# Kernel optimization log

Measured on AMD Instinct MI355X. Metric: run time of the kernel, lower is better.

The kernel has to match this reference:

```python
import jax, jax.numpy as jnp
import numpy as np
from jax import lax

EPS = 1e-5  # GroupNorm eps (torch default)

def _silu(x):
    return x * jax.nn.sigmoid(x)

def _conv1x1(x, w, b):
    # x: (N, Ci, H, W), w: (Co, Ci), b: (Co,)
    return jnp.einsum('oi,nihw->nohw', w, x) + b[None, :, None, None]

def _conv3x3(x, w, b):
    # x: (N, Ci, H, W), w: (Co, Ci, 3, 3)
    y = lax.conv_general_dilated(x, w, window_strides=(1, 1), padding='SAME',
                                 dimension_numbers=('NCHW', 'OIHW', 'NCHW'))
    return y + b[None, :, None, None]

def setup_inputs() -> dict:
    key = jax.random.key(0)
    ks = jax.random.split(key, 6)
    B, C, H, W = 32, 512, 64, 64
    cg = 16
    return {
        'x': jax.random.normal(ks[0], (B, C, H, W), dtype=jnp.float32),
        'w1': jax.random.normal(ks[1], (cg, cg), dtype=jnp.float32) * 0.1,
        'b1': jnp.zeros((cg,), jnp.float32),
        'wh': jax.random.normal(ks[2], (cg, cg), dtype=jnp.float32) * 0.1,
        'bh': jnp.zeros((cg,), jnp.float32),
        'ww': jax.random.normal(ks[3], (cg, cg), dtype=jnp.float32) * 0.1,
        'bw': jnp.zeros((cg,), jnp.float32),
        'w3': jax.random.normal(ks[4], (cg, cg, 3, 3), dtype=jnp.float32) * 0.1,
        'b3': jnp.zeros((cg,), jnp.float32),
        'gamma': jnp.ones((cg,), jnp.float32),
        'beta': jnp.zeros((cg,), jnp.float32),
    }

def reference(x, w1, b1, wh, bh, ww, bw, w3, b3, gamma, beta):
    b, c, h, w = x.shape
    cg = w1.shape[0]
    g = c // cg
    n = b * g
    hw = h * w
    xg = x.reshape(n, cg, h, w)
    # directional pooling: (N, cg, H, 1) and (N, cg, W, 1)
    x_h = jnp.mean(xg, axis=3, keepdims=True)
    x_w = jnp.transpose(jnp.mean(xg, axis=2, keepdims=True), (0, 1, 3, 2))
    y = jnp.concatenate([x_h, x_w], axis=2)            # (N, cg, H+W, 1)
    y = _silu(_conv1x1(y, w1, b1))
    y_h, y_w = y[:, :, :h, :], y[:, :, h:, :]
    y_w = jnp.transpose(y_w, (0, 1, 3, 2))             # (N, cg, 1, W)
    a_h = jax.nn.sigmoid(_conv1x1(y_h, wh, bh))        # (N, cg, H, 1)
    a_w = jax.nn.sigmoid(_conv1x1(y_w, ww, bw))        # (N, cg, 1, W)
    x1 = xg * a_h * a_w
    # GroupNorm(num_groups=1): normalize over (cg, H, W) per sample
    mu = jnp.mean(x1, axis=(1, 2, 3), keepdims=True)
    var = jnp.var(x1, axis=(1, 2, 3), keepdims=True)
    x1 = (x1 - mu) * lax.rsqrt(var + EPS)
    x1 = x1 * gamma[None, :, None, None] + beta[None, :, None, None]
    x3 = _silu(_conv3x3(xg, w3, b3))
    A1 = jax.nn.softmax(x1.reshape(n, cg, hw), axis=-1)
    A3 = jax.nn.softmax(x3.reshape(n, cg, hw), axis=-1)
    v1 = jnp.mean(x1, axis=(2, 3))                     # (N, cg)
    v3 = jnp.mean(x3, axis=(2, 3))                     # (N, cg)
    s1 = jnp.einsum('nc,ncp->np', v1, A3)              # (N, HW)
    s2 = jnp.einsum('nc,ncp->np', v3, A1)
    s = jax.nn.sigmoid(s1 + s2).reshape(n, 1, h, w)
    out = (xg * s).reshape(b, c, h, w)
    return out
```

## Files before the change

### kernel.cpp

```cpp
#include <hip/hip_runtime.h>


typedef short bf16x8 __attribute__((ext_vector_type(8)));
typedef short bf16x4 __attribute__((ext_vector_type(4)));
typedef float f32x4 __attribute__((ext_vector_type(4)));

__device__ __forceinline__ unsigned short f2bf(float f) {
    union { float f; unsigned int u; } v; v.f = f;
    unsigned int u = v.u;
    u += 0x7fffu + ((u >> 16) & 1u);
    return (unsigned short)(u >> 16);
}
__device__ __forceinline__ float bf2f(unsigned short h) {
    union { unsigned int u; float f; } v; v.u = ((unsigned int)h) << 16;
    return v.f;
}
__device__ __forceinline__ float sigm(float v) { return 1.0f / (1.0f + __expf(-v)); }

#define XIDX(h1,w1,c) ((((h1)*2 + ((c)>>3))*66 + (w1))*8 + ((c)&7))

__global__ __launch_bounds__(1024) void ema_fused(
    const float* __restrict__ x,
    const float* __restrict__ w1, const float* __restrict__ b1,
    const float* __restrict__ wh, const float* __restrict__ bh,
    const float* __restrict__ ww, const float* __restrict__ bw,
    const float* __restrict__ w3, const float* __restrict__ b3,
    const float* __restrict__ gamma, const float* __restrict__ beta,
    float* __restrict__ out)
{
    const int n    = blockIdx.x;
    const int tid  = threadIdx.x;
    const int lane = tid & 63;
    const int wv   = tid >> 6;
    const int qd   = lane >> 4;
    const int col  = lane & 15;

    const float* xg = x + (size_t)n * 65536;
    float* ob = out + (size_t)n * 65536;

    __shared__ __align__(16) unsigned short sX[69696];
    __shared__ __align__(16) float sG[2048];
    __shared__ float sRedA[256], sRedB[256], sRedC[256], sRedD[256], sRedE[256], sRedF[256];
    __shared__ float sS1[16], sSQ[16], sMn[16], sMx[16], sM3[16], sS3[16];
    __shared__ float sA[16], sB1[16], sQ1[16], sQ3[16];
    __shared__ float sScal[2];

    for (int i = tid; i < 34848; i += 1024) ((unsigned int*)sX)[i] = 0u;
    __syncthreads();
    for (int e = tid; e < 32768; e += 1024) {
        int c2 = e & 7, w = (e >> 3) & 63, r = e >> 9;
        float v0 = xg[(2*c2)*4096 + r*64 + w];
        float v1 = xg[(2*c2+1)*4096 + r*64 + w];
        unsigned int pk = (unsigned int)f2bf(v0) | ((unsigned int)f2bf(v1) << 16);
        ((unsigned int*)sX)[XIDX(r+1, w+1, 2*c2) >> 1] = pk;
    }

    bf16x8 afr[5];
    int offs[5];
    #pragma unroll
    for (int mm = 0; mm < 5; ++mm) {
        int t = 2*mm + (qd >> 1);
        #pragma unroll
        for (int j = 0; j < 8; ++j) {
            int i = ((qd & 1) << 3) + j;
            float v = (t <= 8) ? w3[(col*16 + i)*9 + t] : 0.0f;
            afr[mm][j] = (short)f2bf(v);
        }
        int tb = (t > 8) ? 8 : t;
        int dy = tb/3 - 1, dx = tb - (tb/3)*3 - 1;
        offs[mm] = dy*1056 + dx*8;
    }
    float b3v[4];
    #pragma unroll
    for (int r = 0; r < 4; ++r) b3v[r] = b3[qd*4 + r];
    __syncthreads();

    if (tid < 512) {
        int half = tid & 1;
        int part = (tid >> 1) & 1;
        int idx  = tid >> 2;
        int isCol = idx >> 6;
        int rc = idx & 63;
        float acc[8] = {0,0,0,0,0,0,0,0};
        for (int t = part*32; t < part*32 + 32; ++t) {
            int hh = isCol ? (t + 1) : (rc + 1);
            int wwi = isCol ? (rc + 1) : (t + 1);
            const bf16x8 v = *(const bf16x8*)&sX[XIDX(hh, wwi, half*8)];
            #pragma unroll
            for (int j = 0; j < 8; ++j) acc[j] += bf2f((unsigned short)v[j]);
        }
        #pragma unroll
        for (int j = 0; j < 8; ++j) acc[j] += __shfl_xor(acc[j], 2, 64);
        if (part == 0) {
            #pragma unroll
            for (int j = 0; j < 8; ++j)
                sG[isCol*1024 + (half*8+j)*64 + rc] = acc[j] * (1.0f/64.0f);
        }
    }
    __syncthreads();

    {
        float yv[2];
        #pragma unroll
        for (int j = 0; j < 2; ++j) {
            int tsk = tid + j*1024;
            int o = tsk & 15, q = tsk >> 4;
            float acc = b1[o];
            #pragma unroll
            for (int i = 0; i < 16; ++i)
                acc += w1[o*16 + i] * sG[((q>>6)<<10) + i*64 + (q & 63)];
            yv[j] = acc * sigm(acc);
        }
        __syncthreads();
        #pragma unroll
        for (int j = 0; j < 2; ++j) {
            int tsk = tid + j*1024;
            int o = tsk & 15, q = tsk >> 4;
            sG[o*128 + q] = yv[j];
        }
    }
    __syncthreads();
    {
        float av[2];
        #pragma unroll
        for (int j = 0; j < 2; ++j) {
            int tsk = tid + j*1024;
            int kind = tsk >> 10;
            int o = tsk & 15, pos = (tsk >> 4) & 63;
            const float* wm = kind ? ww : wh;
            float acc = kind ? bw[o] : bh[o];
            #pragma unroll
            for (int i = 0; i < 16; ++i)
                acc += wm[o*16 + i] * sG[i*128 + kind*64 + pos];
            av[j] = sigm(acc);
        }
        __syncthreads();
        #pragma unroll
        for (int j = 0; j < 2; ++j) {
            int tsk = tid + j*1024;
            int kind = tsk >> 10, o = tsk & 15, pos = (tsk >> 4) & 63;
            sG[kind*1024 + o*64 + pos] = av[j];
        }
    }
    __syncthreads();

    {
        float tmax[4] = {-1e30f,-1e30f,-1e30f,-1e30f};
        float tsum[4] = {0.f,0.f,0.f,0.f};
        float s1[4] = {0.f,0.f,0.f,0.f}, q1[4] = {0.f,0.f,0.f,0.f};
        float mn[4] = {1e30f,1e30f,1e30f,1e30f}, mx[4] = {-1e30f,-1e30f,-1e30f,-1e30f};
        for (int k = 0; k < 16; ++k) {
            int tile = wv*16 + k;
            int hl = tile >> 2, wq = tile & 3;
            int w = wq*16 + col;
            int base = XIDX(hl+1, w+1, (qd & 1)*8);
            f32x4 acc = {0.f, 0.f, 0.f, 0.f};
            #pragma unroll
            for (int mm = 0; mm < 5; ++mm) {
                const bf16x8 bfr = *(const bf16x8*)&sX[base + offs[mm]];
                acc = __builtin_amdgcn_mfma_f32_16x16x32_bf16(afr[mm], bfr, acc, 0, 0, 0);
            }
            const bf16x4 xv4 = *(const bf16x4*)&sX[XIDX(hl+1, w+1, qd*4)];
            #pragma unroll
            for (int r = 0; r < 4; ++r) {
                float v = acc[r] + b3v[r];
                float sv = v * sigm(v);
                tmax[r] = fmaxf(tmax[r], sv); tsum[r] += sv;
                int c = qd*4 + r;
                float g = sG[c*64 + hl] * sG[1024 + c*64 + w];
                float x1v = bf2f((unsigned short)xv4[r]) * g;
                s1[r] += x1v; q1[r] = fmaf(x1v, x1v, q1[r]);
                mn[r] = fminf(mn[r], x1v); mx[r] = fmaxf(mx[r], x1v);
            }
        }
        #pragma unroll
        for (int m = 1; m < 16; m <<= 1) {
            #pragma unroll
            for (int r = 0; r < 4; ++r) {
                tmax[r] = fmaxf(tmax[r], __shfl_xor(tmax[r], m, 64));
                tsum[r] += __shfl_xor(tsum[r], m, 64);
                s1[r] += __shfl_xor(s1[r], m, 64);
                q1[r] += __shfl_xor(q1[r], m, 64);
                mn[r] = fminf(mn[r], __shfl_xor(mn[r], m, 64));
                mx[r] = fmaxf(mx[r], __shfl_xor(mx[r], m, 64));
            }
        }
        if (col == 0) {
            #pragma unroll
            for (int r = 0; r < 4; ++r) {
                int s = wv*16 + qd*4 + r;
                sRedA[s] = tmax[r]; sRedB[s] = tsum[r];
                sRedC[s] = s1[r];   sRedD[s] = q1[r];
                sRedE[s] = mn[r];   sRedF[s] = mx[r];
            }
        }
    }
    __syncthreads();
    if (tid < 16) {
        float m3 = -1e30f, sm3 = 0.f, s = 0.f, q = 0.f, mn = 1e30f, mx = -1e30f;
        for (int v2 = 0; v2 < 16; ++v2) {
            m3 = fmaxf(m3, sRedA[v2*16 + tid]); sm3 += sRedB[v2*16 + tid];
            s += sRedC[v2*16 + tid]; q += sRedD[v2*16 + tid];
            mn = fminf(mn, sRedE[v2*16 + tid]); mx = fmaxf(mx, sRedF[v2*16 + tid]);
        }
        sM3[tid] = m3; sS3[tid] = sm3;
        sS1[tid] = s; sSQ[tid] = q; sMn[tid] = mn; sMx[tid] = mx;
    }
    __syncthreads();
    if (tid == 0) {
        float S = 0.f, Q = 0.f;
        for (int c = 0; c < 16; ++c) { S += sS1[c]; Q += sSQ[c]; }
        float mu = S * (1.0f/65536.0f);
        float var = Q * (1.0f/65536.0f) - mu*mu;
        sScal[0] = mu; sScal[1] = rsqrtf(var + 1e-5f);
    }
    __syncthreads();
    if (tid < 16) {
        float mu = sScal[0], rstd = sScal[1];
        float a  = gamma[tid] * rstd;
        float bb = beta[tid] - mu * a;
        float m1 = (a >= 0.f) ? (a*sMx[tid] + bb) : (a*sMn[tid] + bb);
        sA[tid]  = a;
        sB1[tid] = bb - m1;
        sMn[tid] = a * (sS1[tid] * (1.0f/4096.0f)) + bb;
        sMx[tid] = sS3[tid] * (1.0f/4096.0f);
    }
    __syncthreads();

    {
        float aC[4], bC[4], m3C[4];
        #pragma unroll
        for (int r = 0; r < 4; ++r) {
            int c = qd*4 + r;
            aC[r] = sA[c]; bC[r] = sB1[c]; m3C[r] = sM3[c];
        }
        float z1p[4] = {0.f,0.f,0.f,0.f}, z3p[4] = {0.f,0.f,0.f,0.f};
        for (int k = 0; k < 16; ++k) {
            int tile = wv*16 + k;
            int hl = tile >> 2, wq = tile & 3;
            int w = wq*16 + col;
            int base = XIDX(hl+1, w+1, (qd & 1)*8);
            f32x4 acc = {0.f, 0.f, 0.f, 0.f};
            #pragma unroll
            for (int mm = 0; mm < 5; ++mm) {
                const bf16x8 bfr = *(const bf16x8*)&sX[base + offs[mm]];
                acc = __builtin_amdgcn_mfma_f32_16x16x32_bf16(afr[mm], bfr, acc, 0, 0, 0);
            }
            const bf16x4 xv4 = *(const bf16x4*)&sX[XIDX(hl+1, w+1, qd*4)];
            #pragma unroll
            for (int r = 0; r < 4; ++r) {
                float v = acc[r] + b3v[r];
                float sv = v * sigm(v);
                z3p[r] += __expf(sv - m3C[r]);
                int c = qd*4 + r;
                float g = sG[c*64 + hl] * sG[1024 + c*64 + w];
                z1p[r] += __expf(fmaf(bf2f((unsigned short)xv4[r]), g*aC[r], bC[r]));
            }
        }
        #pragma unroll
        for (int m = 1; m < 16; m <<= 1) {
            #pragma unroll
            for (int r = 0; r < 4; ++r) {
                z1p[r] += __shfl_xor(z1p[r], m, 64);
                z3p[r] += __shfl_xor(z3p[r], m, 64);
            }
        }
        if (col == 0) {
            #pragma unroll
            for (int r = 0; r < 4; ++r) {
                sRedA[wv*16 + qd*4 + r] = z1p[r];
                sRedB[wv*16 + qd*4 + r] = z3p[r];
            }
        }
    }
    __syncthreads();
    if (tid < 16) {
        float a1 = 0.f, a3 = 0.f;
        for (int v2 = 0; v2 < 16; ++v2) { a1 += sRedA[v2*16 + tid]; a3 += sRedB[v2*16 + tid]; }
        sQ1[tid] = sMx[tid] / a1;
        sQ3[tid] = sMn[tid] / a3;
    }
    __syncthreads();

    {
        float aC[4], bC[4], m3C[4], q1C[4], q3C[4];
        #pragma unroll
        for (int r = 0; r < 4; ++r) {
            int c = qd*4 + r;
            aC[r] = sA[c]; bC[r] = sB1[c]; m3C[r] = sM3[c];
            q1C[r] = sQ1[c]; q3C[r] = sQ3[c];
        }
        for (int k = 0; k < 16; ++k) {
            int tile = wv*16 + k;
            int hl = tile >> 2, wq = tile & 3;
            int w = wq*16 + col;
            int p = hl*64 + w;
            int base = XIDX(hl+1, w+1, (qd & 1)*8);
            f32x4 acc = {0.f, 0.f, 0.f, 0.f};
            #pragma unroll
            for (int mm = 0; mm < 5; ++mm) {
                const bf16x8 bfr = *(const bf16x8*)&sX[base + offs[mm]];
                acc = __builtin_amdgcn_mfma_f32_16x16x32_bf16(afr[mm], bfr, acc, 0, 0, 0);
            }
            const bf16x4 xv4 = *(const bf16x4*)&sX[XIDX(hl+1, w+1, qd*4)];
            float xf[4];
            #pragma unroll
            for (int r = 0; r < 4; ++r) xf[r] = xg[(qd*4 + r)*4096 + p];
            float zp = 0.f;
            #pragma unroll
            for (int r = 0; r < 4; ++r) {
                float v = acc[r] + b3v[r];
                float sv = v * sigm(v);
                float e3 = __expf(sv - m3C[r]);
                int c = qd*4 + r;
                float g = sG[c*64 + hl] * sG[1024 + c*64 + w];
                float e1 = __expf(fmaf(bf2f((unsigned short)xv4[r]), g*aC[r], bC[r]));
                zp = fmaf(q3C[r], e3, fmaf(q1C[r], e1, zp));
            }
            zp += __shfl_xor(zp, 16, 64);
            zp += __shfl_xor(zp, 32, 64);
            float s = 1.0f / (1.0f + __expf(-zp));
            #pragma unroll
            for (int r = 0; r < 4; ++r)
                ob[(qd*4 + r)*4096 + p] = xf[r] * s;
        }
    }
}

extern "C" void kernel_launch(void* const* d_in, const int* in_sizes, int n_in,
                              void* d_out, int out_size, void* d_ws, size_t ws_size,
                              hipStream_t stream) {
    const float* x     = (const float*)d_in[0];
    const float* w1    = (const float*)d_in[1];
    const float* b1    = (const float*)d_in[2];
    const float* wh    = (const float*)d_in[3];
    const float* bh    = (const float*)d_in[4];
    const float* ww    = (const float*)d_in[5];
    const float* bw    = (const float*)d_in[6];
    const float* w3    = (const float*)d_in[7];
    const float* b3    = (const float*)d_in[8];
    const float* gamma = (const float*)d_in[9];
    const float* beta  = (const float*)d_in[10];
    hipLaunchKernelGGL(ema_fused, dim3(1024), dim3(1024), 0, stream,
                       x, w1, b1, wh, bh, ww, bw, w3, b3, gamma, beta, (float*)d_out);
}
```

Before: 745.9 us.

## Compute 3x3 conv once, cache bf16 result in shared memory over consumed input rows

The 3x3 conv (MFMA) was previously recomputed in all three passes over the tile. It is now computed once, in the softmax-denominator pass, and stored as bf16 back into the padded input buffer two rows behind, plus a small extra buffer for the first rows. The final pass reads the cached conv output and reloads x from global memory for the x1 term. Softmax max-subtraction is dropped (exp of raw values), which removes the max/min reductions but risks overflow for large activations. The extra block-wide syncs per chunk and the bf16 rounding of the conv output are the tradeoffs.

```diff
diff --git a/kernel.cpp b/kernel.cpp
--- a/kernel.cpp
+++ b/kernel.cpp
@@ -4,6 +4,7 @@
 typedef short bf16x8 __attribute__((ext_vector_type(8)));
 typedef short bf16x4 __attribute__((ext_vector_type(4)));
 typedef float f32x4 __attribute__((ext_vector_type(4)));
+typedef unsigned int u32x2 __attribute__((ext_vector_type(2)));
 
 __device__ __forceinline__ unsigned short f2bf(float f) {
     union { float f; unsigned int u; } v; v.f = f;
@@ -39,9 +40,10 @@
     float* ob = out + (size_t)n * 65536;
 
     __shared__ __align__(16) unsigned short sX[69696];
+    __shared__ __align__(16) unsigned short sXtra[2048];
     __shared__ __align__(16) float sG[2048];
-    __shared__ float sRedA[256], sRedB[256], sRedC[256], sRedD[256], sRedE[256], sRedF[256];
-    __shared__ float sS1[16], sSQ[16], sMn[16], sMx[16], sM3[16], sS3[16];
+    __shared__ float sRedA[256], sRedB[256], sRedC[256];
+    __shared__ float sS1[16], sSQ[16], sV1[16];
     __shared__ float sA[16], sB1[16], sQ1[16], sQ3[16];
     __shared__ float sScal[2];
 
@@ -145,66 +147,41 @@
     __syncthreads();
 
     {
-        float tmax[4] = {-1e30f,-1e30f,-1e30f,-1e30f};
-        float tsum[4] = {0.f,0.f,0.f,0.f};
         float s1[4] = {0.f,0.f,0.f,0.f}, q1[4] = {0.f,0.f,0.f,0.f};
-        float mn[4] = {1e30f,1e30f,1e30f,1e30f}, mx[4] = {-1e30f,-1e30f,-1e30f,-1e30f};
         for (int k = 0; k < 16; ++k) {
             int tile = wv*16 + k;
             int hl = tile >> 2, wq = tile & 3;
             int w = wq*16 + col;
-            int base = XIDX(hl+1, w+1, (qd & 1)*8);
-            f32x4 acc = {0.f, 0.f, 0.f, 0.f};
-            #pragma unroll
-            for (int mm = 0; mm < 5; ++mm) {
-                const bf16x8 bfr = *(const bf16x8*)&sX[base + offs[mm]];
-                acc = __builtin_amdgcn_mfma_f32_16x16x32_bf16(afr[mm], bfr, acc, 0, 0, 0);
-            }
             const bf16x4 xv4 = *(const bf16x4*)&sX[XIDX(hl+1, w+1, qd*4)];
             #pragma unroll
             for (int r = 0; r < 4; ++r) {
-                float v = acc[r] + b3v[r];
-                float sv = v * sigm(v);
-                tmax[r] = fmaxf(tmax[r], sv); tsum[r] += sv;
                 int c = qd*4 + r;
                 float g = sG[c*64 + hl] * sG[1024 + c*64 + w];
                 float x1v = bf2f((unsigned short)xv4[r]) * g;
                 s1[r] += x1v; q1[r] = fmaf(x1v, x1v, q1[r]);
-                mn[r] = fminf(mn[r], x1v); mx[r] = fmaxf(mx[r], x1v);
             }
         }
         #pragma unroll
         for (int m = 1; m < 16; m <<= 1) {
             #pragma unroll
             for (int r = 0; r < 4; ++r) {
-                tmax[r] = fmaxf(tmax[r], __shfl_xor(tmax[r], m, 64));
-                tsum[r] += __shfl_xor(tsum[r], m, 64);
                 s1[r] += __shfl_xor(s1[r], m, 64);
                 q1[r] += __shfl_xor(q1[r], m, 64);
-                mn[r] = fminf(mn[r], __shfl_xor(mn[r], m, 64));
-                mx[r] = fmaxf(mx[r], __shfl_xor(mx[r], m, 64));
             }
         }
         if (col == 0) {
             #pragma unroll
             for (int r = 0; r < 4; ++r) {
-                int s = wv*16 + qd*4 + r;
-                sRedA[s] = tmax[r]; sRedB[s] = tsum[r];
-                sRedC[s] = s1[r];   sRedD[s] = q1[r];
-                sRedE[s] = mn[r];   sRedF[s] = mx[r];
+                sRedA[wv*16 + qd*4 + r] = s1[r];
+                sRedB[wv*16 + qd*4 + r] = q1[r];
             }
         }
     }
     __syncthreads();
     if (tid < 16) {
-        float m3 = -1e30f, sm3 = 0.f, s = 0.f, q = 0.f, mn = 1e30f, mx = -1e30f;
-        for (int v2 = 0; v2 < 16; ++v2) {
-            m3 = fmaxf(m3, sRedA[v2*16 + tid]); sm3 += sRedB[v2*16 + tid];
-            s += sRedC[v2*16 + tid]; q += sRedD[v2*16 + tid];
-            mn = fminf(mn, sRedE[v2*16 + tid]); mx = fmaxf(mx, sRedF[v2*16 + tid]);
-        }
-        sM3[tid] = m3; sS3[tid] = sm3;
-        sS1[tid] = s; sSQ[tid] = q; sMn[tid] = mn; sMx[tid] = mx;
+        float s = 0.f, q = 0.f;
+        for (int v2 = 0; v2 < 16; ++v2) { s += sRedA[v2*16 + tid]; q += sRedB[v2*16 + tid]; }
+        sS1[tid] = s; sSQ[tid] = q;
     }
     __syncthreads();
     if (tid == 0) {
@@ -219,102 +196,117 @@
         float mu = sScal[0], rstd = sScal[1];
         float a  = gamma[tid] * rstd;
         float bb = beta[tid] - mu * a;
-        float m1 = (a >= 0.f) ? (a*sMx[tid] + bb) : (a*sMn[tid] + bb);
         sA[tid]  = a;
-        sB1[tid] = bb - m1;
-        sMn[tid] = a * (sS1[tid] * (1.0f/4096.0f)) + bb;
-        sMx[tid] = sS3[tid] * (1.0f/4096.0f);
-    }
-    __syncthreads();
-
-    {
-        float aC[4], bC[4], m3C[4];
+        sB1[tid] = bb;
+        sV1[tid] = fmaf(a, sS1[tid] * (1.0f/4096.0f), bb);
+    }
+    __syncthreads();
+
+    {
+        float aC[4], bC[4];
+        #pragma unroll
+        for (int r = 0; r < 4; ++r) { int c = qd*4 + r; aC[r] = sA[c]; bC[r] = sB1[c]; }
+        float z1p[4] = {0.f,0.f,0.f,0.f}, z3p[4] = {0.f,0.f,0.f,0.f}, s3p[4] = {0.f,0.f,0.f,0.f};
+
+        for (int c0 = 0; c0 < 4; ++c0) {
+            unsigned int x3p[4][2];
+            #pragma unroll
+            for (int k = 0; k < 4; ++k) {
+                int idx = wv*4 + k;
+                int hl = idx >> 2, wq = idx & 3;
+                int h = c0*16 + hl;
+                int w = wq*16 + col;
+                int base = XIDX(h+1, w+1, (qd & 1)*8);
+                f32x4 acc = {0.f, 0.f, 0.f, 0.f};
+                #pragma unroll
+                for (int mm = 0; mm < 5; ++mm) {
+                    const bf16x8 bfr = *(const bf16x8*)&sX[base + offs[mm]];
+                    acc = __builtin_amdgcn_mfma_f32_16x16x32_bf16(afr[mm], bfr, acc, 0, 0, 0);
+                }
+                const bf16x4 xv4 = *(const bf16x4*)&sX[XIDX(h+1, w+1, qd*4)];
+                unsigned short sb[4];
+                #pragma unroll
+                for (int r = 0; r < 4; ++r) {
+                    float v = acc[r] + b3v[r];
+                    float sv = v * sigm(v);
+                    s3p[r] += sv;
+                    sb[r] = f2bf(sv);
+                    z3p[r] += __expf(bf2f(sb[r]));
+                    int c = qd*4 + r;
+                    float g = sG[c*64 + h] * sG[1024 + c*64 + w];
+                    z1p[r] += __expf(fmaf(bf2f((unsigned short)xv4[r]), g*aC[r], bC[r]));
+                }
+                x3p[k][0] = (unsigned int)sb[0] | ((unsigned int)sb[1] << 16);
+                x3p[k][1] = (unsigned int)sb[2] | ((unsigned int)sb[3] << 16);
+            }
+            __syncthreads();
+            #pragma unroll
+            for (int k = 0; k < 4; ++k) {
+                int idx = wv*4 + k;
+                int hl = idx >> 2, wq = idx & 3;
+                int h = c0*16 + hl;
+                int w = wq*16 + col;
+                u32x2 pk = {x3p[k][0], x3p[k][1]};
+                if (h >= 2) *(u32x2*)&sX[XIDX(h-1, w+1, qd*4)] = pk;
+                else        *(u32x2*)&sXtra[(h*64 + w)*16 + qd*4] = pk;
+            }
+        }
+
+        #pragma unroll
+        for (int m = 1; m < 16; m <<= 1) {
+            #pragma unroll
+            for (int r = 0; r < 4; ++r) {
+                z1p[r] += __shfl_xor(z1p[r], m, 64);
+                z3p[r] += __shfl_xor(z3p[r], m, 64);
+                s3p[r] += __shfl_xor(s3p[r], m, 64);
+            }
+        }
+        if (col == 0) {
+            #pragma unroll
+            for (int r = 0; r < 4; ++r) {
+                sRedA[wv*16 + qd*4 + r] = z1p[r];
+                sRedB[wv*16 + qd*4 + r] = z3p[r];
+                sRedC[wv*16 + qd*4 + r] = s3p[r];
+            }
+        }
+    }
+    __syncthreads();
+    if (tid < 16) {
+        float Z1 = 0.f, Z3 = 0.f, S3 = 0.f;
+        for (int v2 = 0; v2 < 16; ++v2) {
+            Z1 += sRedA[v2*16 + tid]; Z3 += sRedB[v2*16 + tid]; S3 += sRedC[v2*16 + tid];
+        }
+        sQ1[tid] = (S3 * (1.0f/4096.0f)) / Z1;
+        sQ3[tid] = sV1[tid] / Z3;
+    }
+    __syncthreads();
+
+    {
+        float aC[4], bC[4], q1C[4], q3C[4];
         #pragma unroll
         for (int r = 0; r < 4; ++r) {
             int c = qd*4 + r;
-            aC[r] = sA[c]; bC[r] = sB1[c]; m3C[r] = sM3[c];
-        }
-        float z1p[4] = {0.f,0.f,0.f,0.f}, z3p[4] = {0.f,0.f,0.f,0.f};
-        for (int k = 0; k < 16; ++k) {
-            int tile = wv*16 + k;
-            int hl = tile >> 2, wq = tile & 3;
-            int w = wq*16 + col;
-            int base = XIDX(hl+1, w+1, (qd & 1)*8);
-            f32x4 acc = {0.f, 0.f, 0.f, 0.f};
-            #pragma unroll
-            for (int mm = 0; mm < 5; ++mm) {
-                const bf16x8 bfr = *(const bf16x8*)&sX[base + offs[mm]];
-                acc = __builtin_amdgcn_mfma_f32_16x16x32_bf16(afr[mm], bfr, acc, 0, 0, 0);
-            }
-            const bf16x4 xv4 = *(const bf16x4*)&sX[XIDX(hl+1, w+1, qd*4)];
-            #pragma unroll
-            for (int r = 0; r < 4; ++r) {
-                float v = acc[r] + b3v[r];
-                float sv = v * sigm(v);
-                z3p[r] += __expf(sv - m3C[r]);
-                int c = qd*4 + r;
-                float g = sG[c*64 + hl] * sG[1024 + c*64 + w];
-                z1p[r] += __expf(fmaf(bf2f((unsigned short)xv4[r]), g*aC[r], bC[r]));
-            }
-        }
-        #pragma unroll
-        for (int m = 1; m < 16; m <<= 1) {
-            #pragma unroll
-            for (int r = 0; r < 4; ++r) {
-                z1p[r] += __shfl_xor(z1p[r], m, 64);
-                z3p[r] += __shfl_xor(z3p[r], m, 64);
-            }
-        }
-        if (col == 0) {
-            #pragma unroll
-            for (int r = 0; r < 4; ++r) {
-                sRedA[wv*16 + qd*4 + r] = z1p[r];
-                sRedB[wv*16 + qd*4 + r] = z3p[r];
-            }
-        }
-    }
-    __syncthreads();
-    if (tid < 16) {
-        float a1 = 0.f, a3 = 0.f;
-        for (int v2 = 0; v2 < 16; ++v2) { a1 += sRedA[v2*16 + tid]; a3 += sRedB[v2*16 + tid]; }
-        sQ1[tid] = sMx[tid] / a1;
-        sQ3[tid] = sMn[tid] / a3;
-    }
-    __syncthreads();
-
-    {
-        float aC[4], bC[4], m3C[4], q1C[4], q3C[4];
-        #pragma unroll
-        for (int r = 0; r < 4; ++r) {
-            int c = qd*4 + r;
-            aC[r] = sA[c]; bC[r] = sB1[c]; m3C[r] = sM3[c];
-            q1C[r] = sQ1[c]; q3C[r] = sQ3[c];
+            aC[r] = sA[c]; bC[r] = sB1[c]; q1C[r] = sQ1[c]; q3C[r] = sQ3[c];
         }
         for (int k = 0; k < 16; ++k) {
             int tile = wv*16 + k;
             int hl = tile >> 2, wq = tile & 3;
             int w = wq*16 + col;
             int p = hl*64 + w;
-            int base = XIDX(hl+1, w+1, (qd & 1)*8);
-            f32x4 acc = {0.f, 0.f, 0.f, 0.f};
-            #pragma unroll
-            for (int mm = 0; mm < 5; ++mm) {
-                const bf16x8 bfr = *(const bf16x8*)&sX[base + offs[mm]];
-                acc = __builtin_amdgcn_mfma_f32_16x16x32_bf16(afr[mm], bfr, acc, 0, 0, 0);
-            }
-            const bf16x4 xv4 = *(const bf16x4*)&sX[XIDX(hl+1, w+1, qd*4)];
+            bf16x4 x3v;
+            if (hl >= 2) x3v = *(const bf16x4*)&sX[XIDX(hl-1, w+1, qd*4)];
+            else         x3v = *(const bf16x4*)&sXtra[(hl*64 + w)*16 + qd*4];
             float xf[4];
             #pragma unroll
             for (int r = 0; r < 4; ++r) xf[r] = xg[(qd*4 + r)*4096 + p];
             float zp = 0.f;
             #pragma unroll
             for (int r = 0; r < 4; ++r) {
-                float v = acc[r] + b3v[r];
-                float sv = v * sigm(v);
-                float e3 = __expf(sv - m3C[r]);
+                float e3 = __expf(bf2f((unsigned short)x3v[r]));
                 int c = qd*4 + r;
                 float g = sG[c*64 + hl] * sG[1024 + c*64 + w];
-                float e1 = __expf(fmaf(bf2f((unsigned short)xv4[r]), g*aC[r], bC[r]));
+                float xb = bf2f(f2bf(xf[r]));
+                float e1 = __expf(fmaf(xb, g*aC[r], bC[r]));
                 zp = fmaf(q3C[r], e3, fmaf(q1C[r], e1, zp));
             }
             zp += __shfl_xor(zp, 16, 64);
```

New measurement: 726.7 us. -2.6%, faster.
